# Kernel optimization log

Hardware: AMD Instinct MI355X
Metric: run time of the kernel (lower is better)

The kernel has to match this reference:

```python
import jax, jax.numpy as jnp
import numpy as np

ALPHA = 1.0
GAMMA = 2.0
LABEL_SMOOTHING = 0.1
CENTER_W = 0.1
B, C = 32768, 1000


def setup_inputs() -> dict:
    key = jax.random.key(0)
    k1, k2 = jax.random.split(key)
    inputs = jax.random.normal(k1, (B, C), dtype=jnp.float32)
    targets = jax.random.randint(k2, (B,), 0, C, dtype=jnp.int64)
    return {"inputs": inputs, "targets": targets}


def reference(inputs, targets):
    n_classes = inputs.shape[1]
    # --- cross entropy with label smoothing (reduction='none') ---
    logp = jax.nn.log_softmax(inputs, axis=-1)                      # [B, C]
    nll = -jnp.take_along_axis(logp, targets[:, None], axis=1)[:, 0]  # [B]
    smooth = -jnp.mean(logp, axis=-1)                               # [B]
    ce = (1.0 - LABEL_SMOOTHING) * nll + LABEL_SMOOTHING * smooth
    # --- focal weighting ---
    pt = jnp.exp(-ce)
    focal = ALPHA * (1.0 - pt) ** GAMMA * ce                        # [B]
    # --- center loss (single-pass segment reduce, no per-class loop) ---
    # torch code sets centers[b, t_b] = mean_i{inputs[i, t_b] : targets[i]==t_b},
    # zero elsewhere.  sum((x - centers)^2) expands to three cheap reductions.
    gathered = jnp.take_along_axis(inputs, targets[:, None], axis=1)[:, 0]  # [B]
    sums = jax.ops.segment_sum(gathered, targets, num_segments=n_classes)
    counts = jax.ops.segment_sum(jnp.ones_like(gathered), targets,
                                 num_segments=n_classes)
    class_mean = jnp.where(counts > 0, sums / jnp.maximum(counts, 1.0), 0.0)
    m = class_mean[targets]                                          # [B]
    n_elems = inputs.shape[0] * inputs.shape[1]
    center = (jnp.sum(inputs ** 2) - 2.0 * jnp.sum(gathered * m)
              + jnp.sum(m ** 2)) / n_elems                           # scalar
    total = focal + CENTER_W * center                                # broadcast scalar
    return total.mean()
```

## Files before the change

### kernel.cpp

```cpp
#include <hip/hip_runtime.h>
#include <cmath>

#define BB 32768
#define CC 1000
#define NF4 250
#define WPB 8
#define NBLK (BB / WPB)

__device__ __forceinline__ float wave_reduce_sum(float v) {
  #pragma unroll
  for (int m = 32; m >= 1; m >>= 1) v += __shfl_xor(v, m, 64);
  return v;
}

__global__ __launch_bounds__(512) void hfl_rows(
    const float* __restrict__ x, const int* __restrict__ tgt,
    float* __restrict__ class_sum, float* __restrict__ class_cnt,
    float2* __restrict__ partials) {
  const int wave = threadIdx.x >> 6;
  const int lane = threadIdx.x & 63;
  const int row  = blockIdx.x * WPB + wave;

  const float4* rp = reinterpret_cast<const float4*>(x + (size_t)row * CC);
  const int t = tgt[row];
  const float g = x[(size_t)row * CC + t];

  float4 v0 = rp[lane];
  float4 v1 = rp[64 + lane];
  float4 v2 = rp[128 + lane];
  const bool val3 = (192 + lane) < NF4;
  float4 v3 = {0.f, 0.f, 0.f, 0.f};
  if (val3) v3 = rp[192 + lane];

  float se = 0.f, s = 0.f, s2 = 0.f;
  se += __expf(v0.x) + __expf(v0.y) + __expf(v0.z) + __expf(v0.w);
  s  += (v0.x + v0.y) + (v0.z + v0.w);
  s2 += (v0.x * v0.x + v0.y * v0.y) + (v0.z * v0.z + v0.w * v0.w);
  se += __expf(v1.x) + __expf(v1.y) + __expf(v1.z) + __expf(v1.w);
  s  += (v1.x + v1.y) + (v1.z + v1.w);
  s2 += (v1.x * v1.x + v1.y * v1.y) + (v1.z * v1.z + v1.w * v1.w);
  se += __expf(v2.x) + __expf(v2.y) + __expf(v2.z) + __expf(v2.w);
  s  += (v2.x + v2.y) + (v2.z + v2.w);
  s2 += (v2.x * v2.x + v2.y * v2.y) + (v2.z * v2.z + v2.w * v2.w);
  if (val3) {
    se += __expf(v3.x) + __expf(v3.y) + __expf(v3.z) + __expf(v3.w);
    s  += (v3.x + v3.y) + (v3.z + v3.w);
    s2 += (v3.x * v3.x + v3.y * v3.y) + (v3.z * v3.z + v3.w * v3.w);
  }

  se = wave_reduce_sum(se);
  s  = wave_reduce_sum(s);
  s2 = wave_reduce_sum(s2);

  __shared__ float2 sh[WPB];
  if (lane == 0) {
    const float lse = __logf(se);
    const float ce  = lse - 0.9f * g - 0.1f * (s * (1.0f / CC));
    const float pt  = __expf(-ce);
    const float omp = 1.0f - pt;
    sh[wave] = make_float2(omp * omp * ce, s2);
    atomicAdd(&class_sum[t], g);
    atomicAdd(&class_cnt[t], 1.0f);
  }
  __syncthreads();
  if (threadIdx.x == 0) {
    float f = 0.f, q = 0.f;
    #pragma unroll
    for (int w = 0; w < WPB; ++w) { f += sh[w].x; q += sh[w].y; }
    partials[blockIdx.x] = make_float2(f, q);
  }
}

__global__ __launch_bounds__(1024) void hfl_final(
    const float* __restrict__ class_sum, const float* __restrict__ class_cnt,
    const float2* __restrict__ partials, float* __restrict__ out) {
  const int tid = threadIdx.x;
  float f = 0.f, s2 = 0.f, ct = 0.f;
  #pragma unroll
  for (int i = 0; i < NBLK / 1024; ++i) {
    const float2 p = partials[tid + i * 1024];
    f += p.x; s2 += p.y;
  }
  if (tid < CC) {
    const float cnt = class_cnt[tid];
    if (cnt > 0.f) {
      const float sm = class_sum[tid];
      ct = sm * sm / cnt;
    }
  }
  f  = wave_reduce_sum(f);
  s2 = wave_reduce_sum(s2);
  ct = wave_reduce_sum(ct);

  __shared__ float shf[16], shs[16], shc[16];
  const int wave = tid >> 6, lane = tid & 63;
  if (lane == 0) { shf[wave] = f; shs[wave] = s2; shc[wave] = ct; }
  __syncthreads();
  if (tid == 0) {
    float F = 0.f, S = 0.f, T = 0.f;
    #pragma unroll
    for (int w = 0; w < 16; ++w) { F += shf[w]; S += shs[w]; T += shc[w]; }
    const float center = (S - T) * (1.0f / ((float)BB * (float)CC));
    out[0] = F * (1.0f / (float)BB) + 0.1f * center;
  }
}

extern "C" void kernel_launch(void* const* d_in, const int* in_sizes, int n_in,
                              void* d_out, int out_size, void* d_ws, size_t ws_size,
                              hipStream_t stream) {
  const float* x   = (const float*)d_in[0];
  const int*   tgt = (const int*)d_in[1];
  float* out = (float*)d_out;

  float*  class_sum = (float*)d_ws;
  float*  class_cnt = (float*)((char*)d_ws + 4096);
  float2* partials  = (float2*)((char*)d_ws + 8192);

  hipMemsetAsync(d_ws, 0, 8192, stream);

  hfl_rows<<<NBLK, 512, 0, stream>>>(x, tgt, class_sum, class_cnt, partials);
  hfl_final<<<1, 1024, 0, stream>>>(class_sum, class_cnt, partials, out);
}
```

Measured before the change: 33.91 us.

## Replace global per-class atomics with LDS segment reduce in final kernel

The row kernel now writes each row's gathered target logit to a workspace array instead of issuing two global atomicAdds per row into class sum and count buffers. The single-block final kernel rebuilds the per-class sums and counts with shared-memory atomics over all rows. This removes the global atomic contention and the memset launch. The cost is that the serial final block now reads targets and gathered values for all 32768 rows.

Measured after the change: 109.1 us. +221.7%, slower.

```diff
diff --git a/kernel.cpp b/kernel.cpp
--- a/kernel.cpp
+++ b/kernel.cpp
@@ -15,8 +15,7 @@
 
 __global__ __launch_bounds__(512) void hfl_rows(
     const float* __restrict__ x, const int* __restrict__ tgt,
-    float* __restrict__ class_sum, float* __restrict__ class_cnt,
-    float2* __restrict__ partials) {
+    float* __restrict__ gvals, float2* __restrict__ partials) {
   const int wave = threadIdx.x >> 6;
   const int lane = threadIdx.x & 63;
   const int row  = blockIdx.x * WPB + wave;
@@ -53,16 +52,19 @@
   s2 = wave_reduce_sum(s2);
 
   __shared__ float2 sh[WPB];
+  __shared__ float shg[WPB];
   if (lane == 0) {
     const float lse = __logf(se);
     const float ce  = lse - 0.9f * g - 0.1f * (s * (1.0f / CC));
     const float pt  = __expf(-ce);
     const float omp = 1.0f - pt;
-    sh[wave] = make_float2(omp * omp * ce, s2);
-    atomicAdd(&class_sum[t], g);
-    atomicAdd(&class_cnt[t], 1.0f);
+    sh[wave]  = make_float2(omp * omp * ce, s2);
+    shg[wave] = g;
   }
   __syncthreads();
+  if (threadIdx.x < WPB) {
+    gvals[blockIdx.x * WPB + threadIdx.x] = shg[threadIdx.x];
+  }
   if (threadIdx.x == 0) {
     float f = 0.f, q = 0.f;
     #pragma unroll
@@ -72,21 +74,32 @@
 }
 
 __global__ __launch_bounds__(1024) void hfl_final(
-    const float* __restrict__ class_sum, const float* __restrict__ class_cnt,
+    const int* __restrict__ tgt, const float* __restrict__ gvals,
     const float2* __restrict__ partials, float* __restrict__ out) {
+  __shared__ float ls[CC];
+  __shared__ float lc[CC];
   const int tid = threadIdx.x;
-  float f = 0.f, s2 = 0.f, ct = 0.f;
+  if (tid < CC) { ls[tid] = 0.f; lc[tid] = 0.f; }
+  __syncthreads();
+
+  float f = 0.f, s2 = 0.f;
   #pragma unroll
   for (int i = 0; i < NBLK / 1024; ++i) {
     const float2 p = partials[tid + i * 1024];
     f += p.x; s2 += p.y;
   }
+  #pragma unroll 4
+  for (int i = tid; i < BB; i += 1024) {
+    const int t = tgt[i];
+    atomicAdd(&ls[t], gvals[i]);
+    atomicAdd(&lc[t], 1.0f);
+  }
+  __syncthreads();
+
+  float ct = 0.f;
   if (tid < CC) {
-    const float cnt = class_cnt[tid];
-    if (cnt > 0.f) {
-      const float sm = class_sum[tid];
-      ct = sm * sm / cnt;
-    }
+    const float c = lc[tid];
+    if (c > 0.f) ct = ls[tid] * ls[tid] / c;
   }
   f  = wave_reduce_sum(f);
   s2 = wave_reduce_sum(s2);
@@ -112,12 +125,9 @@
   const int*   tgt = (const int*)d_in[1];
   float* out = (float*)d_out;
 
-  float*  class_sum = (float*)d_ws;
-  float*  class_cnt = (float*)((char*)d_ws + 4096);
-  float2* partials  = (float2*)((char*)d_ws + 8192);
+  float*  gvals    = (float*)d_ws;
+  float2* partials = (float2*)((char*)d_ws + BB * 4);
 
-  hipMemsetAsync(d_ws, 0, 8192, stream);
-
-  hfl_rows<<<NBLK, 512, 0, stream>>>(x, tgt, class_sum, class_cnt, partials);
-  hfl_final<<<1, 1024, 0, stream>>>(class_sum, class_cnt, partials, out);
+  hfl_rows<<<NBLK, 512, 0, stream>>>(x, tgt, gvals, partials);
+  hfl_final<<<1, 1024, 0, stream>>>(tgt, gvals, partials, out);
 }
```

## Move class histogram to shared-memory kernel and drop memset launch

Applied to the files above, without the earlier changes.

Removes the separate memset by having block 0 of the row kernel zero the workspace, and takes the per-row global atomics to class_sum/class_cnt out of the row kernel. A new 32-block histogram kernel regathers target logits, accumulates per-class sums and counts in LDS, flushes them with global atomics, reduces the partials, and uses a last-block counter to compute the final output. The aim is to cut launch overhead and global atomic contention. In exchange it re-reads the gathered elements, and zeroing inside block 0 relies on that block running before other blocks' atomics only in the second kernel, which stream ordering guarantees.

After: 36.13 us. 6.5% more time.

```diff
diff --git a/kernel.cpp b/kernel.cpp
--- a/kernel.cpp
+++ b/kernel.cpp
@@ -6,6 +6,7 @@
 #define NF4 250
 #define WPB 8
 #define NBLK (BB / WPB)
+#define HBLK 32
 
 __device__ __forceinline__ float wave_reduce_sum(float v) {
   #pragma unroll
@@ -15,8 +16,12 @@
 
 __global__ __launch_bounds__(512) void hfl_rows(
     const float* __restrict__ x, const int* __restrict__ tgt,
-    float* __restrict__ class_sum, float* __restrict__ class_cnt,
+    float* __restrict__ zero_region,
     float2* __restrict__ partials) {
+  if (blockIdx.x == 0) {
+    #pragma unroll
+    for (int i = threadIdx.x; i < 2056; i += 512) zero_region[i] = 0.f;
+  }
   const int wave = threadIdx.x >> 6;
   const int lane = threadIdx.x & 63;
   const int row  = blockIdx.x * WPB + wave;
@@ -59,8 +64,6 @@
     const float pt  = __expf(-ce);
     const float omp = 1.0f - pt;
     sh[wave] = make_float2(omp * omp * ce, s2);
-    atomicAdd(&class_sum[t], g);
-    atomicAdd(&class_cnt[t], 1.0f);
   }
   __syncthreads();
   if (threadIdx.x == 0) {
@@ -71,37 +74,70 @@
   }
 }
 
-__global__ __launch_bounds__(1024) void hfl_final(
-    const float* __restrict__ class_sum, const float* __restrict__ class_cnt,
-    const float2* __restrict__ partials, float* __restrict__ out) {
-  const int tid = threadIdx.x;
-  float f = 0.f, s2 = 0.f, ct = 0.f;
-  #pragma unroll
-  for (int i = 0; i < NBLK / 1024; ++i) {
-    const float2 p = partials[tid + i * 1024];
-    f += p.x; s2 += p.y;
-  }
-  if (tid < CC) {
-    const float cnt = class_cnt[tid];
-    if (cnt > 0.f) {
-      const float sm = class_sum[tid];
-      ct = sm * sm / cnt;
-    }
+__global__ __launch_bounds__(1024) void hfl_hist(
+    const float* __restrict__ x, const int* __restrict__ tgt,
+    const float2* __restrict__ partials,
+    float* __restrict__ class_sum, float* __restrict__ class_cnt,
+    float* __restrict__ acc,
+    unsigned int* __restrict__ counter,
+    float* __restrict__ out) {
+  __shared__ float ls[CC], lc[CC];
+  const int tid  = threadIdx.x;
+  const int wave = tid >> 6, lane = tid & 63;
+  if (tid < CC) { ls[tid] = 0.f; lc[tid] = 0.f; }
+  __syncthreads();
+
+  const int i = blockIdx.x * 1024 + tid;
+  const int t = tgt[i];
+  const float g = x[(size_t)i * CC + t];
+  atomicAdd(&ls[t], g);
+  atomicAdd(&lc[t], 1.0f);
+
+  float f = 0.f, s2 = 0.f;
+  if (tid < 2 * 64) {
+    const float2 p = partials[blockIdx.x * 128 + tid];
+    f = p.x; s2 = p.y;
   }
   f  = wave_reduce_sum(f);
   s2 = wave_reduce_sum(s2);
-  ct = wave_reduce_sum(ct);
+  if (wave < 2 && lane == 0) {
+    atomicAdd(&acc[0], f);
+    atomicAdd(&acc[1], s2);
+  }
+  __syncthreads();
+  if (tid < CC) {
+    atomicAdd(&class_sum[tid], ls[tid]);
+    atomicAdd(&class_cnt[tid], lc[tid]);
+  }
 
-  __shared__ float shf[16], shs[16], shc[16];
-  const int wave = tid >> 6, lane = tid & 63;
-  if (lane == 0) { shf[wave] = f; shs[wave] = s2; shc[wave] = ct; }
+  __shared__ int is_last;
   __syncthreads();
   if (tid == 0) {
-    float F = 0.f, S = 0.f, T = 0.f;
+    __threadfence();
+    is_last = (atomicAdd(counter, 1u) == HBLK - 1);
+  }
+  __syncthreads();
+  if (!is_last) return;
+  __threadfence();
+
+  float ct = 0.f;
+  if (tid < CC) {
+    const float c = class_cnt[tid];
+    if (c > 0.f) {
+      const float sm = class_sum[tid];
+      ct = sm * sm / c;
+    }
+  }
+  ct = wave_reduce_sum(ct);
+  __shared__ float shc[16];
+  if (lane == 0) shc[wave] = ct;
+  __syncthreads();
+  if (tid == 0) {
+    float T = 0.f;
     #pragma unroll
-    for (int w = 0; w < 16; ++w) { F += shf[w]; S += shs[w]; T += shc[w]; }
-    const float center = (S - T) * (1.0f / ((float)BB * (float)CC));
-    out[0] = F * (1.0f / (float)BB) + 0.1f * center;
+    for (int w = 0; w < 16; ++w) T += shc[w];
+    const float center = (acc[1] - T) * (1.0f / ((float)BB * (float)CC));
+    out[0] = acc[0] * (1.0f / (float)BB) + 0.1f * center;
   }
 }
 
@@ -112,12 +148,13 @@
   const int*   tgt = (const int*)d_in[1];
   float* out = (float*)d_out;
 
-  float*  class_sum = (float*)d_ws;
-  float*  class_cnt = (float*)((char*)d_ws + 4096);
-  float2* partials  = (float2*)((char*)d_ws + 8192);
+  float*        class_sum = (float*)d_ws;
+  float*        class_cnt = (float*)((char*)d_ws + 4096);
+  float*        acc       = (float*)((char*)d_ws + 8192);
+  unsigned int* counter   = (unsigned int*)((char*)d_ws + 8200);
+  float2*       partials  = (float2*)((char*)d_ws + 8448);
 
-  hipMemsetAsync(d_ws, 0, 8192, stream);
-
-  hfl_rows<<<NBLK, 512, 0, stream>>>(x, tgt, class_sum, class_cnt, partials);
-  hfl_final<<<1, 1024, 0, stream>>>(class_sum, class_cnt, partials, out);
+  hfl_rows<<<NBLK, 512, 0, stream>>>(x, tgt, (float*)d_ws, partials);
+  hfl_hist<<<HBLK, 1024, 0, stream>>>(x, tgt, partials, class_sum, class_cnt,
+                                      acc, counter, out);
 }
```

## Fuse final reduction into row kernel via last-block atomic counter

Applied to the files above, without the earlier changes.

Merges the two-kernel pipeline into one kernel. Each block atomically adds its focal and squared-sum partials to global accumulators and bumps a counter, and the last block to finish computes the class-mean term and writes the output. This removes the second launch and the partials round-trip. In exchange it adds global atomics per block, and it relies on atomic visibility with no explicit fence before the last block reads class_sum and acc. The target-element load is also moved after the row loads.

After: 124.5 us. 3.67x slower.

```diff
diff --git a/kernel.cpp b/kernel.cpp
--- a/kernel.cpp
+++ b/kernel.cpp
@@ -13,17 +13,18 @@
   return v;
 }
 
-__global__ __launch_bounds__(512) void hfl_rows(
+__global__ __launch_bounds__(512, 8) void hfl_fused(
     const float* __restrict__ x, const int* __restrict__ tgt,
     float* __restrict__ class_sum, float* __restrict__ class_cnt,
-    float2* __restrict__ partials) {
+    float* __restrict__ acc,
+    unsigned int* __restrict__ counter,
+    float* __restrict__ out) {
   const int wave = threadIdx.x >> 6;
   const int lane = threadIdx.x & 63;
   const int row  = blockIdx.x * WPB + wave;
 
   const float4* rp = reinterpret_cast<const float4*>(x + (size_t)row * CC);
   const int t = tgt[row];
-  const float g = x[(size_t)row * CC + t];
 
   float4 v0 = rp[lane];
   float4 v1 = rp[64 + lane];
@@ -31,6 +32,7 @@
   const bool val3 = (192 + lane) < NF4;
   float4 v3 = {0.f, 0.f, 0.f, 0.f};
   if (val3) v3 = rp[192 + lane];
+  const float g = x[(size_t)row * CC + t];
 
   float se = 0.f, s = 0.f, s2 = 0.f;
   se += __expf(v0.x) + __expf(v0.y) + __expf(v0.z) + __expf(v0.w);
@@ -53,53 +55,51 @@
   s2 = wave_reduce_sum(s2);
 
   __shared__ float2 sh[WPB];
+  __shared__ int last_flag;
   if (lane == 0) {
     const float lse = __logf(se);
     const float ce  = lse - 0.9f * g - 0.1f * (s * (1.0f / CC));
     const float pt  = __expf(-ce);
     const float omp = 1.0f - pt;
     sh[wave] = make_float2(omp * omp * ce, s2);
-    atomicAdd(&class_sum[t], g);
-    atomicAdd(&class_cnt[t], 1.0f);
+    const float r0 = atomicAdd(&class_sum[t], g);
+    const float r1 = atomicAdd(&class_cnt[t], 1.0f);
+    asm volatile("" :: "v"(r0), "v"(r1));
   }
   __syncthreads();
+
   if (threadIdx.x == 0) {
     float f = 0.f, q = 0.f;
     #pragma unroll
     for (int w = 0; w < WPB; ++w) { f += sh[w].x; q += sh[w].y; }
-    partials[blockIdx.x] = make_float2(f, q);
+    const float a0 = atomicAdd(&acc[0], f);
+    const float a1 = atomicAdd(&acc[1], q);
+    asm volatile("" :: "v"(a0), "v"(a1));
+    const unsigned int old = atomicAdd(counter, 1u);
+    last_flag = ((old & (NBLK - 1)) == (NBLK - 1));
   }
-}
+  __syncthreads();
+  if (!last_flag) return;
 
-__global__ __launch_bounds__(1024) void hfl_final(
-    const float* __restrict__ class_sum, const float* __restrict__ class_cnt,
-    const float2* __restrict__ partials, float* __restrict__ out) {
-  const int tid = threadIdx.x;
-  float f = 0.f, s2 = 0.f, ct = 0.f;
-  #pragma unroll
-  for (int i = 0; i < NBLK / 1024; ++i) {
-    const float2 p = partials[tid + i * 1024];
-    f += p.x; s2 += p.y;
+  float ct = 0.f;
+  if (threadIdx.x < 250) {
+    const float4 sm = reinterpret_cast<const float4*>(class_sum)[threadIdx.x];
+    const float4 cn = reinterpret_cast<const float4*>(class_cnt)[threadIdx.x];
+    if (cn.x > 0.f) ct += sm.x * sm.x / cn.x;
+    if (cn.y > 0.f) ct += sm.y * sm.y / cn.y;
+    if (cn.z > 0.f) ct += sm.z * sm.z / cn.z;
+    if (cn.w > 0.f) ct += sm.w * sm.w / cn.w;
   }
-  if (tid < CC) {
-    const float cnt = class_cnt[tid];
-    if (cnt > 0.f) {
-      const float sm = class_sum[tid];
-      ct = sm * sm / cnt;
-    }
-  }
-  f  = wave_reduce_sum(f);
-  s2 = wave_reduce_sum(s2);
   ct = wave_reduce_sum(ct);
-
-  __shared__ float shf[16], shs[16], shc[16];
-  const int wave = tid >> 6, lane = tid & 63;
-  if (lane == 0) { shf[wave] = f; shs[wave] = s2; shc[wave] = ct; }
+  __shared__ float shc[WPB];
+  if (lane == 0) shc[wave] = ct;
   __syncthreads();
-  if (tid == 0) {
-    float F = 0.f, S = 0.f, T = 0.f;
+  if (threadIdx.x == 0) {
+    float T = 0.f;
     #pragma unroll
-    for (int w = 0; w < 16; ++w) { F += shf[w]; S += shs[w]; T += shc[w]; }
+    for (int w = 0; w < WPB; ++w) T += shc[w];
+    const float F = acc[0];
+    const float S = acc[1];
     const float center = (S - T) * (1.0f / ((float)BB * (float)CC));
     out[0] = F * (1.0f / (float)BB) + 0.1f * center;
   }
@@ -112,12 +112,13 @@
   const int*   tgt = (const int*)d_in[1];
   float* out = (float*)d_out;
 
-  float*  class_sum = (float*)d_ws;
-  float*  class_cnt = (float*)((char*)d_ws + 4096);
-  float2* partials  = (float2*)((char*)d_ws + 8192);
+  float*        class_sum = (float*)d_ws;
+  float*        class_cnt = (float*)((char*)d_ws + 4096);
+  float*        acc       = (float*)((char*)d_ws + 8192);
+  unsigned int* counter   = (unsigned int*)((char*)d_ws + 8256);
 
-  hipMemsetAsync(d_ws, 0, 8192, stream);
+  hipMemsetAsync(d_ws, 0, 8320, stream);
 
-  hfl_rows<<<NBLK, 512, 0, stream>>>(x, tgt, class_sum, class_cnt, partials);
-  hfl_final<<<1, 1024, 0, stream>>>(class_sum, class_cnt, partials, out);
+  hfl_fused<<<NBLK, 512, 0, stream>>>(x, tgt, class_sum, class_cnt,
+                                      acc, counter, out);
 }
```
